# Optimization experiments

Hardware: AMD Instinct MI355X
Metric: run time of the kernel (lower is better)

Reference implementation:

```python
import jax, jax.numpy as jnp
import numpy as np

ROI = 7      # pooled output size
S = 5        # max adaptive samples per bin dim (boxes <= 0.25*120=30px -> ceil(30/7)=5)


def _roi_align(f, boxes):
    """torchvision roi_align, aligned=True, sampling_ratio=-1 (adaptive).
    f: [C,H,W]; boxes: [N,4] normalized xywh. Returns [N,C,ROI,ROI]."""
    C, H, W = f.shape
    fH, fW = jnp.float32(H), jnp.float32(W)
    x1 = boxes[:, 0] * fW - 0.5                 # aligned=True offset
    y1 = boxes[:, 1] * fH - 0.5
    roi_w = boxes[:, 2] * fW
    roi_h = boxes[:, 3] * fH
    bin_w = roi_w / ROI
    bin_h = roi_h / ROI
    gw = jnp.maximum(jnp.ceil(roi_w / ROI), 1.0)   # adaptive grid counts [N]
    gh = jnp.maximum(jnp.ceil(roi_h / ROI), 1.0)
    ph = jnp.arange(ROI, dtype=jnp.float32)
    s = jnp.arange(S, dtype=jnp.float32)
    # sample coords [N, ROI, S]
    ys = y1[:, None, None] + ph[None, :, None] * bin_h[:, None, None] \
         + (s[None, None, :] + 0.5) * bin_h[:, None, None] / gh[:, None, None]
    xs = x1[:, None, None] + ph[None, :, None] * bin_w[:, None, None] \
         + (s[None, None, :] + 0.5) * bin_w[:, None, None] / gw[:, None, None]
    # broadcast to [N, ROI, ROI, S, S]
    y = ys[:, :, None, :, None]
    x = xs[:, None, :, None, :]
    m = ((s[None, None, None, :, None] < gh[:, None, None, None, None]) &
         (s[None, None, None, None, :] < gw[:, None, None, None, None]))
    valid = (y > -1.0) & (y < fH) & (x > -1.0) & (x < fW)
    yc = jnp.clip(y, 0.0, fH - 1.0)
    xc = jnp.clip(x, 0.0, fW - 1.0)
    y0 = jnp.floor(yc).astype(jnp.int32)
    x0 = jnp.floor(xc).astype(jnp.int32)
    yh = jnp.minimum(y0 + 1, H - 1)
    xh = jnp.minimum(x0 + 1, W - 1)
    ly = yc - y0.astype(jnp.float32); hy = 1.0 - ly
    lx = xc - x0.astype(jnp.float32); hx = 1.0 - lx
    scale = (valid & m).astype(f.dtype)
    y = jnp.broadcast_to(y0 * 0, (boxes.shape[0], ROI, ROI, S, S))  # shape anchor (unused)
    w00 = (hy * hx * scale)[None]
    w01 = (hy * lx * scale)[None]
    w10 = (ly * hx * scale)[None]
    w11 = (ly * lx * scale)[None]
    # gathered values: [C, N, ROI, ROI, S, S]
    vals = (w00 * f[:, y0, x0] + w01 * f[:, y0, xh] +
            w10 * f[:, yh, x0] + w11 * f[:, yh, xh])
    count = (gh * gw)[None, :, None, None]
    pooled = vals.sum(axis=(-1, -2)) / count        # [C, N, ROI, ROI]
    return pooled.transpose(1, 0, 2, 3)              # [N, C, ROI, ROI]


def setup_inputs() -> dict:
    key = jax.random.key(0)
    k = jax.random.split(key, 6)
    features = jax.random.normal(k[0], (1, 128, 120, 120), jnp.float32)
    u = jax.random.uniform(k[1], (512, 4), jnp.float32)
    boxes = jnp.stack([u[:, 0] * 0.7, u[:, 1] * 0.7,
                       0.05 + 0.2 * u[:, 2], 0.05 + 0.2 * u[:, 3]], axis=1)
    d_in = 128 * ROI * ROI  # 6272
    W1 = jax.random.normal(k[2], (d_in, 512), jnp.float32) / np.float32(np.sqrt(d_in))
    b1 = jax.random.normal(k[3], (512,), jnp.float32) * 0.01
    W2 = jax.random.normal(k[4], (512, 256), jnp.float32) / np.float32(np.sqrt(512))
    b2 = jax.random.normal(k[5], (256,), jnp.float32) * 0.01
    return {"features": features, "boxes": boxes, "W1": W1, "b1": b1, "W2": W2, "b2": b2}


def reference(features, boxes, W1, b1, W2, b2):
    roi = _roi_align(features[0], boxes)             # [N,128,7,7]
    flat = roi.reshape(roi.shape[0], -1)             # [N,6272] channel-major like torch .view
    h = jax.nn.relu(flat @ W1 + b1)                  # dropout in eval mode = identity
    return h @ W2 + b2                               # [N,256]
```

## Files before the change

### kernel.cpp

```cpp
#include <hip/hip_runtime.h>
#include <hip/hip_bf16.h>
#include <stdint.h>

#define DI __device__ __forceinline__

typedef __attribute__((ext_vector_type(8))) short short8;
typedef __attribute__((ext_vector_type(4))) float f32x4;

constexpr int CH   = 128;
constexpr int FH   = 120;
constexpr int FW   = 120;
constexpr int NBOX = 512;
constexpr int KDIM = 49 * 128;
constexpr int D1   = 512;
constexpr int D2   = 256;
constexpr int SPLITS = 14;
constexpr int KC     = KDIM / SPLITS;

DI float bf2f(uint32_t u16) { union { uint32_t i; float f; } v; v.i = u16 << 16; return v.f; }
DI float bf2f_hi(uint32_t u) { union { uint32_t i; float f; } v; v.i = u & 0xffff0000u; return v.f; }
DI uint16_t f2bf(float f) {
    __hip_bfloat16 h = __float2bfloat16(f);
    union { __hip_bfloat16 h; uint16_t u; } v; v.h = h; return v.u;
}
DI f32x4 sp4(float s) { f32x4 r; r.x = s; r.y = s; r.z = s; r.w = s; return r; }
DI f32x4 up4(uint2 q) {
    f32x4 r;
    r.x = bf2f(q.x & 0xffffu); r.y = bf2f_hi(q.x);
    r.z = bf2f(q.y & 0xffffu); r.w = bf2f_hi(q.y);
    return r;
}

__global__ __launch_bounds__(256) void k_preft(const float* __restrict__ f,
                                               uint32_t* __restrict__ ft) {
    __shared__ float lds[30 * 129];
    const int v = blockIdx.x, t = threadIdx.x;
    const int y = v >> 2, x0 = (v & 3) * 30;
    for (int e = t; e < 30 * 128; e += 256) {
        int c = e / 30, x = e - c * 30;
        lds[x * 129 + c] = f[c * (FH * FW) + y * FW + x0 + x];
    }
    __syncthreads();
    for (int e = t; e < 30 * 64; e += 256) {
        int x = e >> 6, cp = e & 63;
        float lo = lds[x * 129 + 2 * cp];
        float hi = lds[x * 129 + 2 * cp + 1];
        ft[(y * FW + x0 + x) * 64 + cp] = (uint32_t)f2bf(lo) | ((uint32_t)f2bf(hi) << 16);
    }
}

template<int GH, int GW>
DI void roi_body(const uint32_t* __restrict__ ft, uint32_t* __restrict__ A,
                 int wid, int lane, int ph, int pw,
                 const float (*__restrict__ tyv)[4], const float (*__restrict__ txv)[4],
                 float cnt) {
#pragma clang fp contract(off)
    const int side = lane >> 5, cl = lane & 31;
    int off[GW];
    float wx[GW];
#pragma unroll
    for (int j = 0; j < GW; ++j) {
        const float* e = txv[pw * 5 + j];
        wx[j]  = side ? e[1] : e[0];
        off[j] = __float_as_int(side ? e[3] : e[2]) + 2 * cl;
    }
    int offy0[GH], offy1[GH];
    float hym[GH], lym[GH];
#pragma unroll
    for (int s = 0; s < GH; ++s) {
        const float* e = tyv[ph * 5 + s];
        hym[s] = e[0]; lym[s] = e[1];
        offy0[s] = __float_as_int(e[2]); offy1[s] = __float_as_int(e[3]);
    }

    f32x4 acc = {0.0f, 0.0f, 0.0f, 0.0f};
    if constexpr (GH * GW <= 12) {
        uint2 q0[GH][GW], q1[GH][GW];
#pragma unroll
        for (int s = 0; s < GH; ++s) {
            const uint32_t* r0 = ft + offy0[s];
            const uint32_t* r1 = ft + offy1[s];
#pragma unroll
            for (int j = 0; j < GW; ++j) {
                q0[s][j] = *(const uint2*)(r0 + off[j]);
                q1[s][j] = *(const uint2*)(r1 + off[j]);
            }
        }
#pragma unroll
        for (int s = 0; s < GH; ++s)
#pragma unroll
            for (int j = 0; j < GW; ++j)
                acc += sp4(hym[s] * wx[j]) * up4(q0[s][j])
                     + sp4(lym[s] * wx[j]) * up4(q1[s][j]);
    } else {
#pragma unroll
        for (int s = 0; s < GH; ++s) {
            const uint32_t* r0 = ft + offy0[s];
            const uint32_t* r1 = ft + offy1[s];
            uint2 q0[GW], q1[GW];
#pragma unroll
            for (int j = 0; j < GW; ++j) {
                q0[j] = *(const uint2*)(r0 + off[j]);
                q1[j] = *(const uint2*)(r1 + off[j]);
            }
#pragma unroll
            for (int j = 0; j < GW; ++j)
                acc += sp4(hym[s] * wx[j]) * up4(q0[j])
                     + sp4(lym[s] * wx[j]) * up4(q1[j]);
        }
    }
    f32x4 tot;
#pragma unroll
    for (int i = 0; i < 4; ++i) tot[i] = acc[i] + __shfl_xor((float)acc[i], 32);
    if (side == 0) {
        uint2 pk;
        pk.x = (uint32_t)f2bf(tot.x / cnt) | ((uint32_t)f2bf(tot.y / cnt) << 16);
        pk.y = (uint32_t)f2bf(tot.z / cnt) | ((uint32_t)f2bf(tot.w / cnt) << 16);
        *(uint2*)(A + (size_t)wid * 64 + 2 * cl) = pk;
    }
}

__global__ __launch_bounds__(256) void k_roi_w(const uint32_t* __restrict__ ft,
                                               const float* __restrict__ boxes,
                                               const float* __restrict__ W1,
                                               const float* __restrict__ W2,
                                               uint32_t* __restrict__ A,
                                               uint16_t* __restrict__ W1rT,
                                               uint16_t* __restrict__ W2T) {
    __shared__ __align__(16) float lds[128 * 33];
    __shared__ __align__(16) float tyv[35][4];
    __shared__ __align__(16) float txv[35][4];
    const int blk = blockIdx.x, t = threadIdx.x;
    if (blk < 6656) {
#pragma clang fp contract(off)
        const int box = blk / 13, quad = blk % 13;
        const float bx = boxes[box * 4 + 0], by = boxes[box * 4 + 1];
        const float bw = boxes[box * 4 + 2], bh = boxes[box * 4 + 3];
        const float x1 = bx * 120.0f - 0.5f;
        const float y1 = by * 120.0f - 0.5f;
        const float roi_w = bw * 120.0f, roi_h = bh * 120.0f;
        const float bin_w = roi_w / 7.0f, bin_h = roi_h / 7.0f;
        const float gwf = fmaxf(ceilf(roi_w / 7.0f), 1.0f);
        const float ghf = fmaxf(ceilf(roi_h / 7.0f), 1.0f);
        const int gwi = (int)gwf, ghi = (int)ghf;
        const float cnt = ghf * gwf;

        if (t < 35) {
            const int ph = t / 5, sy = t % 5;
            float yy = (y1 + (float)ph * bin_h) + ((float)sy + 0.5f) * bin_h / ghf;
            float my = ((yy > -1.0f) && (yy < 120.0f)) ? 1.0f : 0.0f;
            float yc = fminf(fmaxf(yy, 0.0f), 119.0f);
            int y0 = (int)floorf(yc);
            int yh = min(y0 + 1, 119);
            float ly = yc - (float)y0, hy = 1.0f - ly;
            tyv[t][0] = hy * my;
            tyv[t][1] = ly * my;
            tyv[t][2] = __int_as_float(y0 * (FW * 64));
            tyv[t][3] = __int_as_float(yh * (FW * 64));
        } else if (t < 70) {
            const int u = t - 35;
            const int pw = u / 5, sx = u % 5;
            float xx = (x1 + (float)pw * bin_w) + ((float)sx + 0.5f) * bin_w / gwf;
            float mx = ((xx > -1.0f) && (xx < 120.0f)) ? 1.0f : 0.0f;
            float xc = fminf(fmaxf(xx, 0.0f), 119.0f);
            int x0 = (int)floorf(xc);
            int xh = min(x0 + 1, 119);
            float lx = xc - (float)x0, hx = 1.0f - lx;
            txv[u][0] = hx * mx;
            txv[u][1] = lx * mx;
            txv[u][2] = __int_as_float(x0 * 64);
            txv[u][3] = __int_as_float(xh * 64);
        }
        __syncthreads();

        const int w8 = t >> 6, lane = t & 63;
        const int bin = quad * 4 + w8;
        if (bin < 49) {
            const int ph = bin / 7, pw = bin - ph * 7;
            const int wid = box * 49 + bin;
#define RB(GH, GW) roi_body<GH, GW>(ft, A, wid, lane, ph, pw, tyv, txv, cnt)
            switch (ghi * 8 + gwi) {
            case  9: RB(1,1); break; case 10: RB(1,2); break; case 11: RB(1,3); break;
            case 12: RB(1,4); break; case 13: RB(1,5); break;
            case 17: RB(2,1); break; case 18: RB(2,2); break; case 19: RB(2,3); break;
            case 20: RB(2,4); break; case 21: RB(2,5); break;
            case 25: RB(3,1); break; case 26: RB(3,2); break; case 27: RB(3,3); break;
            case 28: RB(3,4); break; case 29: RB(3,5); break;
            case 33: RB(4,1); break; case 34: RB(4,2); break; case 35: RB(4,3); break;
            case 36: RB(4,4); break; case 37: RB(4,5); break;
            case 41: RB(5,1); break; case 42: RB(5,2); break; case 43: RB(5,3); break;
            case 44: RB(5,4); break; default: RB(5,5); break;
            }
#undef RB
        }
    } else if (blk < 7440) {
        const int vb = blk - 6656;
        const int b = vb % 49, j0 = (vb / 49) * 32;
        for (int e = t; e < 4096; e += 256) {
            int ci = e >> 5, jj = e & 31;
            lds[ci * 33 + jj] = W1[(ci * 49 + b) * D1 + j0 + jj];
        }
        __syncthreads();
        for (int e = t; e < 4096; e += 256) {
            int jj = e >> 7, ci = e & 127;
            W1rT[(size_t)(j0 + jj) * KDIM + b * 128 + ci] = f2bf(lds[ci * 33 + jj]);
        }
    } else {
        const int v2 = blk - 7440;
        const int n0 = (v2 & 7) * 32, k0 = (v2 >> 3) * 128;
        for (int e = t; e < 4096; e += 256) {
            int k = e >> 5, nn = e & 31;
            lds[k * 33 + nn] = W2[(k0 + k) * D2 + n0 + nn];
        }
        __syncthreads();
        for (int e = t; e < 4096; e += 256) {
            int nn = e >> 7, k = e & 127;
            W2T[(n0 + nn) * D1 + k0 + k] = f2bf(lds[k * 33 + nn]);
        }
    }
}

__global__ __launch_bounds__(256) void k_gemm1(const uint16_t* __restrict__ A,
                                               const uint16_t* __restrict__ B,
                                               float* __restrict__ P) {
    __shared__ __align__(16) uint16_t As[128 * 32];
    __shared__ __align__(16) uint16_t Bs[128 * 32];
    const int t = threadIdx.x;
    const int lane = t & 63, w = t >> 6;
    const int wr = w >> 1, wc = w & 1;
    const int m0 = blockIdx.x * 128, n0 = blockIdx.y * 128;
    const int kbase = blockIdx.z * KC;

    f32x4 acc[4][4] = {};
    const int kb = lane >> 4, r16 = lane & 15;

    for (int ks = 0; ks < KC / 32; ++ks) {
        const int kk = kbase + ks * 32;
        __syncthreads();
#pragma unroll
        for (int i = 0; i < 2; ++i) {
            int ch = t + 256 * i;
            int row = ch >> 2, c8 = ch & 3;
            int sw = (row >> 1) & 3;
            const uint16_t* ga = A + (size_t)(m0 + row) * KDIM + kk + c8 * 8;
            *(uint4*)&As[row * 32 + (c8 ^ sw) * 8] = *(const uint4*)ga;
            const uint16_t* gb = B + (size_t)(n0 + row) * KDIM + kk + c8 * 8;
            *(uint4*)&Bs[row * 32 + (c8 ^ sw) * 8] = *(const uint4*)gb;
        }
        __syncthreads();

        short8 af[4], bfr[4];
#pragma unroll
        for (int mi = 0; mi < 4; ++mi) {
            int ar = wr * 64 + mi * 16 + r16;
            af[mi] = *(const short8*)&As[ar * 32 + (kb ^ ((ar >> 1) & 3)) * 8];
        }
#pragma unroll
        for (int ni = 0; ni < 4; ++ni) {
            int br = wc * 64 + ni * 16 + r16;
            bfr[ni] = *(const short8*)&Bs[br * 32 + (kb ^ ((br >> 1) & 3)) * 8];
        }
#pragma unroll
        for (int mi = 0; mi < 4; ++mi)
#pragma unroll
            for (int ni = 0; ni < 4; ++ni)
                acc[mi][ni] = __builtin_amdgcn_mfma_f32_16x16x32_bf16(af[mi], bfr[ni], acc[mi][ni], 0, 0, 0);
    }

    float* outp = P + (size_t)blockIdx.z * (D1 * D1);
#pragma unroll
    for (int mi = 0; mi < 4; ++mi)
#pragma unroll
        for (int ni = 0; ni < 4; ++ni) {
            int row = m0 + wr * 64 + mi * 16 + kb * 4;
            int col = n0 + wc * 64 + ni * 16 + r16;
#pragma unroll
            for (int r = 0; r < 4; ++r)
                outp[(size_t)(row + r) * D1 + col] = acc[mi][ni][r];
        }
}

__global__ __launch_bounds__(256) void k_reduce1(const float* __restrict__ P,
                                                 const float* __restrict__ b1,
                                                 uint16_t* __restrict__ Hm) {
    const int e4 = blockIdx.x * 256 + threadIdx.x;
    const f32x4* P4 = (const f32x4*)P;
    f32x4 s = {};
#pragma unroll
    for (int i = 0; i < SPLITS; ++i) s += P4[(size_t)i * (D1 * D1 / 4) + e4];
    const int c4 = (e4 & 127) * 4;
    uint16_t h[4];
#pragma unroll
    for (int j = 0; j < 4; ++j) h[j] = f2bf(fmaxf(s[j] + b1[c4 + j], 0.0f));
    uint2 pk;
    pk.x = (uint32_t)h[0] | ((uint32_t)h[1] << 16);
    pk.y = (uint32_t)h[2] | ((uint32_t)h[3] << 16);
    *(uint2*)&Hm[(size_t)e4 * 4] = pk;
}

__global__ __launch_bounds__(256) void k_gemm2(const uint16_t* __restrict__ Hm,
                                               const uint16_t* __restrict__ W2T,
                                               const float* __restrict__ b2,
                                               float* __restrict__ out) {
    const int wid  = blockIdx.x * 4 + (threadIdx.x >> 6);
    const int lane = threadIdx.x & 63;
    const int mt = wid >> 4, nt = wid & 15;
    const int m0 = mt * 16, n0 = nt * 16;
    const int g = lane >> 4, i = lane & 15;
    f32x4 acc = {};
#pragma unroll
    for (int kk = 0; kk < D1 / 32; ++kk) {
        short8 a = *(const short8*)&Hm[(m0 + i) * D1 + kk * 32 + g * 8];
        short8 b = *(const short8*)&W2T[(n0 + i) * D1 + kk * 32 + g * 8];
        acc = __builtin_amdgcn_mfma_f32_16x16x32_bf16(a, b, acc, 0, 0, 0);
    }
    const float bias = b2[n0 + i];
#pragma unroll
    for (int r = 0; r < 4; ++r)
        out[(size_t)(m0 + g * 4 + r) * D2 + n0 + i] = acc[r] + bias;
}

extern "C" void kernel_launch(void* const* d_in, const int* in_sizes, int n_in,
                              void* d_out, int out_size, void* d_ws, size_t ws_size,
                              hipStream_t stream) {
    const float* f     = (const float*)d_in[0];
    const float* boxes = (const float*)d_in[1];
    const float* W1    = (const float*)d_in[2];
    const float* b1    = (const float*)d_in[3];
    const float* W2    = (const float*)d_in[4];
    const float* b2    = (const float*)d_in[5];
    float* out = (float*)d_out;

    char* p = (char*)d_ws;
    uint32_t* ft   = (uint32_t*)p; p += (size_t)FH * FW * (CH / 2) * 4;
    uint16_t* W1rT = (uint16_t*)p; p += (size_t)D1 * KDIM * 2;
    uint16_t* W2T  = (uint16_t*)p; p += (size_t)D2 * D1 * 2;
    uint16_t* Ar   = (uint16_t*)p; p += (size_t)NBOX * KDIM * 2;
    float*    Pp   = (float*)p;    p += (size_t)SPLITS * D1 * D1 * 4;
    uint16_t* Hm   = (uint16_t*)p; p += (size_t)D1 * D1 * 2;

    k_preft<<<480, 256, 0, stream>>>(f, ft);
    k_roi_w<<<7472, 256, 0, stream>>>(ft, boxes, W1, W2, (uint32_t*)Ar, W1rT, W2T);
    k_gemm1<<<dim3(4, 4, SPLITS), 256, 0, stream>>>(Ar, W1rT, Pp);
    k_reduce1<<<D1 * D1 / 4 / 256, 256, 0, stream>>>(Pp, b1, Hm);
    k_gemm2<<<(D1 / 16) * (D2 / 16) / 4, 256, 0, stream>>>(Hm, W2T, b2, out);
}
```

Measured before the change: 63.11 us.

## Split ROI bilinear corners across lane quarters and shrink GEMM1 tiles to 64x64

The ROI sampling kernel now gives each quarter-wave one bilinear corner (x/y low/high) and has each lane load 8 channels with a 16-byte load. Partial sums are combined with two xor shuffles, where before each lane did two 8-byte loads covering both y rows for 4 channels. GEMM1 tiles drop from 128x128 to 64x64, so the grid grows from 224 to 896 blocks to fill more CUs, and the load addressing is hoisted out of the k loop. In exchange, each GEMM1 block gets less operand reuse and there is more shuffle work per ROI bin.

```diff
diff --git a/kernel.cpp b/kernel.cpp
--- a/kernel.cpp
+++ b/kernel.cpp
@@ -23,13 +23,6 @@
     __hip_bfloat16 h = __float2bfloat16(f);
     union { __hip_bfloat16 h; uint16_t u; } v; v.h = h; return v.u;
 }
-DI f32x4 sp4(float s) { f32x4 r; r.x = s; r.y = s; r.z = s; r.w = s; return r; }
-DI f32x4 up4(uint2 q) {
-    f32x4 r;
-    r.x = bf2f(q.x & 0xffffu); r.y = bf2f_hi(q.x);
-    r.z = bf2f(q.y & 0xffffu); r.w = bf2f_hi(q.y);
-    return r;
-}
 
 __global__ __launch_bounds__(256) void k_preft(const float* __restrict__ f,
                                                uint32_t* __restrict__ ft) {
@@ -51,72 +44,77 @@
 
 template<int GH, int GW>
 DI void roi_body(const uint32_t* __restrict__ ft, uint32_t* __restrict__ A,
-                 int wid, int lane, int ph, int pw,
+                 int wid, int lane,
                  const float (*__restrict__ tyv)[4], const float (*__restrict__ txv)[4],
-                 float cnt) {
+                 int ph, int pw, float cnt) {
 #pragma clang fp contract(off)
-    const int side = lane >> 5, cl = lane & 31;
-    int off[GW];
+    const int q = lane >> 4, cg = lane & 15;
+    const int qx = q & 1, qy = q >> 1;
+    int offx[GW];
     float wx[GW];
 #pragma unroll
     for (int j = 0; j < GW; ++j) {
         const float* e = txv[pw * 5 + j];
-        wx[j]  = side ? e[1] : e[0];
-        off[j] = __float_as_int(side ? e[3] : e[2]) + 2 * cl;
-    }
-    int offy0[GH], offy1[GH];
-    float hym[GH], lym[GH];
+        wx[j]   = qx ? e[1] : e[0];
+        offx[j] = __float_as_int(qx ? e[3] : e[2]) + 4 * cg;
+    }
+    int offy[GH];
+    float wy[GH];
 #pragma unroll
     for (int s = 0; s < GH; ++s) {
         const float* e = tyv[ph * 5 + s];
-        hym[s] = e[0]; lym[s] = e[1];
-        offy0[s] = __float_as_int(e[2]); offy1[s] = __float_as_int(e[3]);
-    }
-
-    f32x4 acc = {0.0f, 0.0f, 0.0f, 0.0f};
+        wy[s]   = qy ? e[1] : e[0];
+        offy[s] = __float_as_int(qy ? e[3] : e[2]);
+    }
+
+    float acc[8] = {};
     if constexpr (GH * GW <= 12) {
-        uint2 q0[GH][GW], q1[GH][GW];
+        uint4 u[GH][GW];
+#pragma unroll
+        for (int s = 0; s < GH; ++s)
+#pragma unroll
+            for (int j = 0; j < GW; ++j)
+                u[s][j] = *(const uint4*)(ft + offy[s] + offx[j]);
+#pragma unroll
+        for (int s = 0; s < GH; ++s)
+#pragma unroll
+            for (int j = 0; j < GW; ++j) {
+                const float w = wy[s] * wx[j];
+                acc[0] += w * bf2f(u[s][j].x & 0xffffu); acc[1] += w * bf2f_hi(u[s][j].x);
+                acc[2] += w * bf2f(u[s][j].y & 0xffffu); acc[3] += w * bf2f_hi(u[s][j].y);
+                acc[4] += w * bf2f(u[s][j].z & 0xffffu); acc[5] += w * bf2f_hi(u[s][j].z);
+                acc[6] += w * bf2f(u[s][j].w & 0xffffu); acc[7] += w * bf2f_hi(u[s][j].w);
+            }
+    } else {
 #pragma unroll
         for (int s = 0; s < GH; ++s) {
-            const uint32_t* r0 = ft + offy0[s];
-            const uint32_t* r1 = ft + offy1[s];
+            uint4 u[GW];
+#pragma unroll
+            for (int j = 0; j < GW; ++j)
+                u[j] = *(const uint4*)(ft + offy[s] + offx[j]);
 #pragma unroll
             for (int j = 0; j < GW; ++j) {
-                q0[s][j] = *(const uint2*)(r0 + off[j]);
-                q1[s][j] = *(const uint2*)(r1 + off[j]);
+                const float w = wy[s] * wx[j];
+                acc[0] += w * bf2f(u[j].x & 0xffffu); acc[1] += w * bf2f_hi(u[j].x);
+                acc[2] += w * bf2f(u[j].y & 0xffffu); acc[3] += w * bf2f_hi(u[j].y);
+                acc[4] += w * bf2f(u[j].z & 0xffffu); acc[5] += w * bf2f_hi(u[j].z);
+                acc[6] += w * bf2f(u[j].w & 0xffffu); acc[7] += w * bf2f_hi(u[j].w);
             }
         }
-#pragma unroll
-        for (int s = 0; s < GH; ++s)
-#pragma unroll
-            for (int j = 0; j < GW; ++j)
-                acc += sp4(hym[s] * wx[j]) * up4(q0[s][j])
-                     + sp4(lym[s] * wx[j]) * up4(q1[s][j]);
-    } else {
-#pragma unroll
-        for (int s = 0; s < GH; ++s) {
-            const uint32_t* r0 = ft + offy0[s];
-            const uint32_t* r1 = ft + offy1[s];
-            uint2 q0[GW], q1[GW];
-#pragma unroll
-            for (int j = 0; j < GW; ++j) {
-                q0[j] = *(const uint2*)(r0 + off[j]);
-                q1[j] = *(const uint2*)(r1 + off[j]);
-            }
-#pragma unroll
-            for (int j = 0; j < GW; ++j)
-                acc += sp4(hym[s] * wx[j]) * up4(q0[j])
-                     + sp4(lym[s] * wx[j]) * up4(q1[j]);
-        }
-    }
-    f32x4 tot;
-#pragma unroll
-    for (int i = 0; i < 4; ++i) tot[i] = acc[i] + __shfl_xor((float)acc[i], 32);
-    if (side == 0) {
-        uint2 pk;
-        pk.x = (uint32_t)f2bf(tot.x / cnt) | ((uint32_t)f2bf(tot.y / cnt) << 16);
-        pk.y = (uint32_t)f2bf(tot.z / cnt) | ((uint32_t)f2bf(tot.w / cnt) << 16);
-        *(uint2*)(A + (size_t)wid * 64 + 2 * cl) = pk;
+    }
+    float tot[8];
+#pragma unroll
+    for (int i = 0; i < 8; ++i) {
+        float v16 = acc[i] + __shfl_xor(acc[i], 16);
+        tot[i] = v16 + __shfl_xor(v16, 32);
+    }
+    if (q == 0) {
+        uint4 pk;
+        pk.x = (uint32_t)f2bf(tot[0] / cnt) | ((uint32_t)f2bf(tot[1] / cnt) << 16);
+        pk.y = (uint32_t)f2bf(tot[2] / cnt) | ((uint32_t)f2bf(tot[3] / cnt) << 16);
+        pk.z = (uint32_t)f2bf(tot[4] / cnt) | ((uint32_t)f2bf(tot[5] / cnt) << 16);
+        pk.w = (uint32_t)f2bf(tot[6] / cnt) | ((uint32_t)f2bf(tot[7] / cnt) << 16);
+        *(uint4*)(A + (size_t)wid * 64 + 4 * cg) = pk;
     }
 }
 
@@ -178,7 +176,7 @@
         if (bin < 49) {
             const int ph = bin / 7, pw = bin - ph * 7;
             const int wid = box * 49 + bin;
-#define RB(GH, GW) roi_body<GH, GW>(ft, A, wid, lane, ph, pw, tyv, txv, cnt)
+#define RB(GH, GW) roi_body<GH, GW>(ft, A, wid, lane, tyv, txv, ph, pw, cnt)
             switch (ghi * 8 + gwi) {
             case  9: RB(1,1); break; case 10: RB(1,2); break; case 11: RB(1,3); break;
             case 12: RB(1,4); break; case 13: RB(1,5); break;
@@ -223,60 +221,56 @@
 __global__ __launch_bounds__(256) void k_gemm1(const uint16_t* __restrict__ A,
                                                const uint16_t* __restrict__ B,
                                                float* __restrict__ P) {
-    __shared__ __align__(16) uint16_t As[128 * 32];
-    __shared__ __align__(16) uint16_t Bs[128 * 32];
+    __shared__ __align__(16) uint16_t As[64 * 32];
+    __shared__ __align__(16) uint16_t Bs[64 * 32];
     const int t = threadIdx.x;
     const int lane = t & 63, w = t >> 6;
     const int wr = w >> 1, wc = w & 1;
-    const int m0 = blockIdx.x * 128, n0 = blockIdx.y * 128;
+    const int m0 = blockIdx.x * 64, n0 = blockIdx.y * 64;
     const int kbase = blockIdx.z * KC;
 
-    f32x4 acc[4][4] = {};
+    f32x4 acc[2][2] = {};
     const int kb = lane >> 4, r16 = lane & 15;
+    const int row = t >> 2, c8 = t & 3;
+    const int ldst = row * 32 + ((c8 ^ ((row >> 1) & 3)) * 8);
+    const uint16_t* ga = A + (size_t)(m0 + row) * KDIM + c8 * 8;
+    const uint16_t* gb = B + (size_t)(n0 + row) * KDIM + c8 * 8;
 
     for (int ks = 0; ks < KC / 32; ++ks) {
         const int kk = kbase + ks * 32;
         __syncthreads();
-#pragma unroll
-        for (int i = 0; i < 2; ++i) {
-            int ch = t + 256 * i;
-            int row = ch >> 2, c8 = ch & 3;
-            int sw = (row >> 1) & 3;
-            const uint16_t* ga = A + (size_t)(m0 + row) * KDIM + kk + c8 * 8;
-            *(uint4*)&As[row * 32 + (c8 ^ sw) * 8] = *(const uint4*)ga;
-            const uint16_t* gb = B + (size_t)(n0 + row) * KDIM + kk + c8 * 8;
-            *(uint4*)&Bs[row * 32 + (c8 ^ sw) * 8] = *(const uint4*)gb;
-        }
-        __syncthreads();
-
-        short8 af[4], bfr[4];
-#pragma unroll
-        for (int mi = 0; mi < 4; ++mi) {
-            int ar = wr * 64 + mi * 16 + r16;
+        *(uint4*)&As[ldst] = *(const uint4*)&ga[kk];
+        *(uint4*)&Bs[ldst] = *(const uint4*)&gb[kk];
+        __syncthreads();
+
+        short8 af[2], bfr[2];
+#pragma unroll
+        for (int mi = 0; mi < 2; ++mi) {
+            int ar = wr * 32 + mi * 16 + r16;
             af[mi] = *(const short8*)&As[ar * 32 + (kb ^ ((ar >> 1) & 3)) * 8];
         }
 #pragma unroll
-        for (int ni = 0; ni < 4; ++ni) {
-            int br = wc * 64 + ni * 16 + r16;
+        for (int ni = 0; ni < 2; ++ni) {
+            int br = wc * 32 + ni * 16 + r16;
             bfr[ni] = *(const short8*)&Bs[br * 32 + (kb ^ ((br >> 1) & 3)) * 8];
         }
 #pragma unroll
-        for (int mi = 0; mi < 4; ++mi)
-#pragma unroll
-            for (int ni = 0; ni < 4; ++ni)
+        for (int mi = 0; mi < 2; ++mi)
+#pragma unroll
+            for (int ni = 0; ni < 2; ++ni)
                 acc[mi][ni] = __builtin_amdgcn_mfma_f32_16x16x32_bf16(af[mi], bfr[ni], acc[mi][ni], 0, 0, 0);
     }
 
     float* outp = P + (size_t)blockIdx.z * (D1 * D1);
 #pragma unroll
-    for (int mi = 0; mi < 4; ++mi)
-#pragma unroll
-        for (int ni = 0; ni < 4; ++ni) {
-            int row = m0 + wr * 64 + mi * 16 + kb * 4;
-            int col = n0 + wc * 64 + ni * 16 + r16;
+    for (int mi = 0; mi < 2; ++mi)
+#pragma unroll
+        for (int ni = 0; ni < 2; ++ni) {
+            int rrow = m0 + wr * 32 + mi * 16 + kb * 4;
+            int ccol = n0 + wc * 32 + ni * 16 + r16;
 #pragma unroll
             for (int r = 0; r < 4; ++r)
-                outp[(size_t)(row + r) * D1 + col] = acc[mi][ni][r];
+                outp[(size_t)(rrow + r) * D1 + ccol] = acc[mi][ni][r];
         }
 }
 
@@ -341,7 +335,7 @@
 
     k_preft<<<480, 256, 0, stream>>>(f, ft);
     k_roi_w<<<7472, 256, 0, stream>>>(ft, boxes, W1, W2, (uint32_t*)Ar, W1rT, W2T);
-    k_gemm1<<<dim3(4, 4, SPLITS), 256, 0, stream>>>(Ar, W1rT, Pp);
+    k_gemm1<<<dim3(8, 8, SPLITS), 256, 0, stream>>>(Ar, W1rT, Pp);
     k_reduce1<<<D1 * D1 / 4 / 256, 256, 0, stream>>>(Pp, b1, Hm);
     k_gemm2<<<(D1 / 16) * (D2 / 16) / 4, 256, 0, stream>>>(Hm, W2T, b2, out);
 }
```

New measurement: 63.03 us. No clear change (-0.1%).
